# Kernel tuning notes

Measured on AMD Instinct MI355X. Metric: run time of the kernel, lower is better.

Reference implementation:

```python
import jax, jax.numpy as jnp
import numpy as np

B, N, C_IN = 8, 2048, 64
NUM_TERMS, NUM_CHANNELS = 3, 64
LN_EPS = 1e-5


def setup_inputs() -> dict:
    key = jax.random.key(0)
    k1, k2, k3 = jax.random.split(key, 3)
    A = jax.random.normal(k1, (B, N, N), dtype=jnp.float32) / jnp.sqrt(N).astype(jnp.float32)
    X = jax.random.normal(k2, (B, N, C_IN), dtype=jnp.float32)
    # xavier_uniform on h of shape [num_terms+1, num_channels, num_nodes]
    fan_in, fan_out = NUM_CHANNELS, N
    bound = float(np.sqrt(6.0 / (fan_in + fan_out)))
    h = jax.random.uniform(k3, (NUM_TERMS + 1, NUM_CHANNELS, N), dtype=jnp.float32,
                           minval=-bound, maxval=bound)
    gamma = jnp.ones((NUM_CHANNELS,), dtype=jnp.float32)
    beta = jnp.zeros((NUM_CHANNELS,), dtype=jnp.float32)
    return {"A": A, "X": X, "h": h, "gamma": gamma, "beta": beta}


def reference(A, X, h, gamma, beta):
    # Original loops compute: Y[b,n,c] = sum_i h[i,c,n] * (A^i @ sum_ch X[...,ch])[b,n]
    num_terms = h.shape[0] - 1
    Xs = X.sum(axis=-1)  # [B, N] -- inner channel loop collapses to a sum

    def step(p, _):
        p_next = jnp.einsum('bmn,bn->bm', A, p)  # A^i @ Xs
        return p_next, p_next

    _, Ps = jax.lax.scan(step, Xs, None, length=num_terms)  # [T, B, N]
    P = jnp.concatenate([Xs[None], Ps], axis=0)  # [T+1, B, N], P[0] = I @ Xs

    Y = jnp.einsum('icn,ibn->bnc', h, P)  # [B, N, C]

    mean = Y.mean(axis=-1, keepdims=True)
    var = Y.var(axis=-1, keepdims=True)
    Yn = (Y - mean) * jax.lax.rsqrt(var + LN_EPS) * gamma + beta
    return jnp.tanh(Yn)
```

## Files before the change

### kernel.cpp

```cpp
#include <hip/hip_runtime.h>
#include <hip/hip_bf16.h>
#include <math.h>

#define BB 8
#define NN 2048
#define C_IN 64
#define NCH 64
#define NTERMS 3
#define LN_EPS 1e-5f

__global__ void xsum_kernel(const float* __restrict__ X, float* __restrict__ Xs) {
    int row  = (blockIdx.x * blockDim.x + threadIdx.x) >> 6;
    int lane = threadIdx.x & 63;
    float v = X[(size_t)row * C_IN + lane];
    #pragma unroll
    for (int off = 32; off > 0; off >>= 1)
        v += __shfl_down(v, off, 64);
    if (lane == 0) Xs[row] = v;
}

#define MV_RPW  2
#define MV_ROWS (4 * MV_RPW)
__global__ __launch_bounds__(256, 4) void matvec_kernel(
        const float* __restrict__ A,
        const float* __restrict__ pin,
        float* __restrict__ pout) {
    const int b    = blockIdx.y;
    const int wave = threadIdx.x >> 6;
    const int lane = threadIdx.x & 63;
    const int m    = blockIdx.x * MV_ROWS + wave * MV_RPW;

    const float4* pin4 = (const float4*)(pin + (size_t)b * NN);
    float4 pr[8];
    #pragma unroll
    for (int j = 0; j < 8; ++j)
        pr[j] = pin4[j * 64 + lane];

    const float4* r0 = (const float4*)(A + (size_t)b * NN * NN + (size_t)m * NN);
    const float4* r1 = r0 + NN / 4;

    float a0 = 0.f, a1 = 0.f;
    #pragma unroll
    for (int it = 0; it < 8; ++it) {
        const int o = it * 64 + lane;
        float4 x0 = r0[o];
        float4 x1 = r1[o];
        a0 += x0.x * pr[it].x + x0.y * pr[it].y + x0.z * pr[it].z + x0.w * pr[it].w;
        a1 += x1.x * pr[it].x + x1.y * pr[it].y + x1.z * pr[it].z + x1.w * pr[it].w;
    }

    #pragma unroll
    for (int off = 32; off > 0; off >>= 1) {
        a0 += __shfl_down(a0, off, 64);
        a1 += __shfl_down(a1, off, 64);
    }
    if (lane == 0) {
        float2 o2 = make_float2(a0, a1);
        *(float2*)(pout + (size_t)b * NN + m) = o2;
    }
}

__global__ __launch_bounds__(256) void combine_kernel(
        const float* __restrict__ h,
        const float* __restrict__ P,
        const float* __restrict__ gamma,
        const float* __restrict__ beta,
        float* __restrict__ out) {
    const int idx  = (blockIdx.x * blockDim.x + threadIdx.x) >> 6;
    const int lane = threadIdx.x & 63;
    const int n    = idx & (NN - 1);

    const float p0 = P[0 * BB * NN + idx];
    const float p1 = P[1 * BB * NN + idx];
    const float p2 = P[2 * BB * NN + idx];
    const float p3 = P[3 * BB * NN + idx];

    float y = h[(size_t)(0 * NCH + lane) * NN + n] * p0
            + h[(size_t)(1 * NCH + lane) * NN + n] * p1
            + h[(size_t)(2 * NCH + lane) * NN + n] * p2
            + h[(size_t)(3 * NCH + lane) * NN + n] * p3;

    float s = y;
    #pragma unroll
    for (int off = 32; off > 0; off >>= 1)
        s += __shfl_xor(s, off, 64);
    const float mean = s * (1.f / NCH);

    float d = y - mean;
    float vs = d * d;
    #pragma unroll
    for (int off = 32; off > 0; off >>= 1)
        vs += __shfl_xor(vs, off, 64);
    const float rstd = rsqrtf(vs * (1.f / NCH) + LN_EPS);

    out[(size_t)idx * NCH + lane] = tanhf(d * rstd * gamma[lane] + beta[lane]);
}

extern "C" void kernel_launch(void* const* d_in, const int* in_sizes, int n_in,
                              void* d_out, int out_size, void* d_ws, size_t ws_size,
                              hipStream_t stream) {
    const float* A     = (const float*)d_in[0];
    const float* X     = (const float*)d_in[1];
    const float* h     = (const float*)d_in[2];
    const float* gamma = (const float*)d_in[3];
    const float* beta  = (const float*)d_in[4];
    float* out = (float*)d_out;

    float* P = (float*)d_ws;

    {
        int rows = BB * NN;
        xsum_kernel<<<rows / 4, 256, 0, stream>>>(X, P);
    }

    dim3 mv_grid(NN / MV_ROWS, BB);
    for (int i = 1; i <= NTERMS; ++i) {
        matvec_kernel<<<mv_grid, 256, 0, stream>>>(
            A, P + (size_t)(i - 1) * BB * NN, P + (size_t)i * BB * NN);
    }

    combine_kernel<<<(BB * NN * 64) / 256, 256, 0, stream>>>(h, P, gamma, beta, out);
}
```

Before: 264.6 us.

## Stage vector in LDS for matvec, one row per wave; regroup combine by node

The matvec kernel now copies the input vector into shared memory once per block, and each wave handles one row of A instead of two. All eight float4 loads of the row are issued up front. This raises the number of blocks and waves in flight and lowers register pressure, which should help hide the memory latency of streaming A. In exchange it adds a block barrier and LDS reads. The combine kernel now runs one block per node n with all 8 batches in it, so the h values for that node are shared across batches through the cache.

```diff
diff --git a/kernel.cpp b/kernel.cpp
--- a/kernel.cpp
+++ b/kernel.cpp
@@ -19,56 +19,53 @@
     if (lane == 0) Xs[row] = v;
 }
 
-#define MV_RPW  2
-#define MV_ROWS (4 * MV_RPW)
-__global__ __launch_bounds__(256, 4) void matvec_kernel(
+__global__ __launch_bounds__(256, 8) void matvec_kernel(
         const float* __restrict__ A,
         const float* __restrict__ pin,
         float* __restrict__ pout) {
-    const int b    = blockIdx.y;
+    __shared__ float p[NN];
+    const int b = blockIdx.y;
+
+    const float4* pin4 = (const float4*)(pin + (size_t)b * NN);
+    float4* p4 = (float4*)p;
+    p4[threadIdx.x]       = pin4[threadIdx.x];
+    p4[threadIdx.x + 256] = pin4[threadIdx.x + 256];
+    __syncthreads();
+
     const int wave = threadIdx.x >> 6;
     const int lane = threadIdx.x & 63;
-    const int m    = blockIdx.x * MV_ROWS + wave * MV_RPW;
+    const int m    = blockIdx.x * 4 + wave;
 
-    const float4* pin4 = (const float4*)(pin + (size_t)b * NN);
-    float4 pr[8];
+    const float4* Ar = (const float4*)(A + (size_t)b * NN * NN + (size_t)m * NN);
+
+    float4 x[8];
     #pragma unroll
     for (int j = 0; j < 8; ++j)
-        pr[j] = pin4[j * 64 + lane];
+        x[j] = Ar[j * 64 + lane];
 
-    const float4* r0 = (const float4*)(A + (size_t)b * NN * NN + (size_t)m * NN);
-    const float4* r1 = r0 + NN / 4;
-
-    float a0 = 0.f, a1 = 0.f;
+    float acc = 0.f;
     #pragma unroll
-    for (int it = 0; it < 8; ++it) {
-        const int o = it * 64 + lane;
-        float4 x0 = r0[o];
-        float4 x1 = r1[o];
-        a0 += x0.x * pr[it].x + x0.y * pr[it].y + x0.z * pr[it].z + x0.w * pr[it].w;
-        a1 += x1.x * pr[it].x + x1.y * pr[it].y + x1.z * pr[it].z + x1.w * pr[it].w;
+    for (int j = 0; j < 8; ++j) {
+        float4 pv = p4[j * 64 + lane];
+        acc += x[j].x * pv.x + x[j].y * pv.y + x[j].z * pv.z + x[j].w * pv.w;
     }
 
     #pragma unroll
-    for (int off = 32; off > 0; off >>= 1) {
-        a0 += __shfl_down(a0, off, 64);
-        a1 += __shfl_down(a1, off, 64);
-    }
-    if (lane == 0) {
-        float2 o2 = make_float2(a0, a1);
-        *(float2*)(pout + (size_t)b * NN + m) = o2;
-    }
+    for (int off = 32; off > 0; off >>= 1)
+        acc += __shfl_down(acc, off, 64);
+    if (lane == 0) pout[(size_t)b * NN + m] = acc;
 }
 
-__global__ __launch_bounds__(256) void combine_kernel(
+__global__ __launch_bounds__(512) void combine_kernel(
         const float* __restrict__ h,
         const float* __restrict__ P,
         const float* __restrict__ gamma,
         const float* __restrict__ beta,
         float* __restrict__ out) {
-    const int idx  = (blockIdx.x * blockDim.x + threadIdx.x) >> 6;
+    const int n    = blockIdx.x;
+    const int b    = threadIdx.x >> 6;
     const int lane = threadIdx.x & 63;
-    const int n    = idx & (NN - 1);
+    const int idx  = b * NN + n;
 
     const float p0 = P[0 * BB * NN + idx];
     const float p1 = P[1 * BB * NN + idx];
@@ -113,11 +110,11 @@
         xsum_kernel<<<rows / 4, 256, 0, stream>>>(X, P);
     }
 
-    dim3 mv_grid(NN / MV_ROWS, BB);
+    dim3 mv_grid(NN / 4, BB);
     for (int i = 1; i <= NTERMS; ++i) {
         matvec_kernel<<<mv_grid, 256, 0, stream>>>(
             A, P + (size_t)(i - 1) * BB * NN, P + (size_t)i * BB * NN);
     }
 
-    combine_kernel<<<(BB * NN * 64) / 256, 256, 0, stream>>>(h, P, gamma, beta, out);
+    combine_kernel<<<NN, 512, 0, stream>>>(h, P, gamma, beta, out);
 }
```

Result: faster. 254.2 us (-3.9%).
